# Kernel tuning notes

Measured on AMD Instinct MI355X. Metric: run time of the kernel, lower is better.

The kernel has to match this reference:

```python
import jax, jax.numpy as jnp
import numpy as np


def _pe(x, y, D):
    # 2D sinusoidal encoding: x in upper half, y in lower half, interleaved sin/cos.
    i = jnp.arange(D // 4, dtype=jnp.float32)
    f = 0.0001 ** (4.0 * i / D)  # (D/4,)

    def half(v):
        a = v[..., None] * f  # (..., D/4)
        return jnp.stack([jnp.sin(a), jnp.cos(a)], axis=-1).reshape(v.shape + (D // 2,))

    return jnp.concatenate([half(x), half(y)], axis=-1)  # (..., D)


def _mlp(x, W1, b1, W2, b2):
    return jax.nn.relu(x @ W1 + b1) @ W2 + b2


def setup_inputs() -> dict:
    key = jax.random.key(0)
    ks = jax.random.split(key, 9)
    B, C, H, S, D = 1024, 64, 21, 3, 1024
    P = S * S * C  # 576
    NS, NSF, NG = 32, 8, 16

    def lin(k, fan_in, fan_out):
        lim = 1.0 / np.sqrt(fan_in)
        return jax.random.uniform(k, (fan_in, fan_out), minval=-lim, maxval=lim, dtype=jnp.float32)

    return {
        "maps": jax.random.normal(ks[0], (B, C, H, H), dtype=jnp.float32),
        "shipyards": jax.random.uniform(ks[1], (B, NS, NSF), dtype=jnp.float32) * 21.0,
        "game_stats": jax.random.normal(ks[2], (B, NG), dtype=jnp.float32),
        "Wp1": lin(ks[3], P, D), "bp1": jnp.zeros((D,), jnp.float32),
        "Wp2": lin(ks[4], D, D), "bp2": jnp.zeros((D,), jnp.float32),
        "Ws1": lin(ks[5], NSF, D), "bs1": jnp.zeros((D,), jnp.float32),
        "Ws2": lin(ks[6], D, D), "bs2": jnp.zeros((D,), jnp.float32),
        "Wg1": lin(ks[7], NG, D), "bg1": jnp.zeros((D,), jnp.float32),
        "Wg2": lin(ks[8], D, D), "bg2": jnp.zeros((D,), jnp.float32),
    }


def reference(maps, shipyards, game_stats, Wp1, bp1, Wp2, bp2,
              Ws1, bs1, Ws2, bs2, Wg1, bg1, Wg2, bg2):
    B, C, H, W = maps.shape
    s = 3  # patch_width
    h, w = H // s, W // s
    D = Wp2.shape[1]
    # Rearrange 'b c (h s1) (w s2) -> b (h w) (s1 s2 c)'
    patches = maps.reshape(B, C, h, s, w, s).transpose(0, 2, 4, 3, 5, 1).reshape(B, h * w, s * s * C)
    emb_p = _mlp(patches, Wp1, bp1, Wp2, bp2)  # (B, 49, D)
    # patch centers: x = 3h+1 (row), y = 3w+1 (col), flattened h-major
    hi, wi = jnp.meshgrid(jnp.arange(h), jnp.arange(w), indexing="ij")
    px = (s * hi + 1).reshape(-1).astype(jnp.float32)
    py = (s * wi + 1).reshape(-1).astype(jnp.float32)
    emb_p = emb_p + _pe(px, py, D)
    emb_s = _mlp(shipyards, Ws1, bs1, Ws2, bs2)  # (B, NS, D)
    # original uses batch element 0's coords for all batches
    emb_s = emb_s + _pe(shipyards[0, :, 0], shipyards[0, :, 1], D)
    emb_g = _mlp(game_stats, Wg1, bg1, Wg2, bg2)[:, None, :]  # (B, 1, D)
    return jnp.concatenate([emb_s, emb_g, emb_p], axis=1)
```

## Files before the change

kernel.cpp:

```cpp
#include <hip/hip_runtime.h>
#include <stdint.h>

typedef __attribute__((ext_vector_type(8))) short bf16x8;
typedef __attribute__((ext_vector_type(4))) float f32x4;

__device__ __forceinline__ unsigned short f2bf(float f) {
  union { float f; uint32_t u; } v; v.f = f;
  uint32_t r = (v.u + 0x7fffu + ((v.u >> 16) & 1u)) >> 16;
  return (unsigned short)r;
}

__device__ __forceinline__ void async16(const void* g, void* l) {
  __builtin_amdgcn_global_load_lds(
      (const __attribute__((address_space(1))) void*)(uintptr_t)g,
      (__attribute__((address_space(3))) void*)(uint32_t)(uintptr_t)l,
      16, 0, 0);
}

__global__ __launch_bounds__(256) void transpose_bf16(
    const float* __restrict__ in, unsigned short* __restrict__ out, int N, int K) {
  __shared__ float tile[32][33];
  int tx = threadIdx.x & 31, ty = threadIdx.x >> 5;
  int n0 = blockIdx.x * 32, k0 = blockIdx.y * 32;
#pragma unroll
  for (int i = 0; i < 32; i += 8)
    tile[ty + i][tx] = in[(size_t)(k0 + ty + i) * N + n0 + tx];
  __syncthreads();
#pragma unroll
  for (int i = 0; i < 32; i += 8)
    out[(size_t)(n0 + ty + i) * K + k0 + tx] = f2bf(tile[tx][ty + i]);
}

__global__ __launch_bounds__(256) void gather_patches(
    const float* __restrict__ maps, unsigned short* __restrict__ P) {
  int bh = blockIdx.x;
  int b = bh / 7, h = bh % 7;
  __shared__ float lds[4032];
  const float* mb = maps + (size_t)b * 64 * 441;
  for (int f = threadIdx.x; f < 4032; f += 256) {
    int c = f / 63, rem = f % 63;
    int s1 = rem / 21, y = rem % 21;
    lds[f] = mb[(size_t)c * 441 + (3 * h + s1) * 21 + y];
  }
  __syncthreads();
  unsigned short* pb = P + ((size_t)b * 49 + (size_t)h * 7) * 576;
#pragma unroll
  for (int w = 0; w < 7; ++w) {
    for (int ep = threadIdx.x; ep < 288; ep += 256) {
      int e = ep * 2;
      int c = e & 63, s2 = (e >> 6) % 3, s1 = e / 192;
      float v0 = lds[c * 63 + s1 * 21 + 3 * w + s2];
      float v1 = lds[(c + 1) * 63 + s1 * 21 + 3 * w + s2];
      ushort2 o; o.x = f2bf(v0); o.y = f2bf(v1);
      *(ushort2*)(pb + (size_t)w * 576 + e) = o;
    }
  }
}

__global__ __launch_bounds__(256) void mlp1_small(
    const float* __restrict__ X, const float* __restrict__ W1,
    const float* __restrict__ b1, unsigned short* __restrict__ H, int K) {
  int t = threadIdx.x;
  size_t r0 = (size_t)blockIdx.x * 16;
  float4 bias = ((const float4*)b1)[t];
  float acc[16][4];
#pragma unroll
  for (int rr = 0; rr < 16; ++rr) {
    acc[rr][0] = bias.x; acc[rr][1] = bias.y; acc[rr][2] = bias.z; acc[rr][3] = bias.w;
  }
  for (int k = 0; k < K; ++k) {
    float4 w = ((const float4*)(W1 + (size_t)k * 1024))[t];
#pragma unroll
    for (int rr = 0; rr < 16; ++rr) {
      float x = X[(r0 + rr) * K + k];
      acc[rr][0] = fmaf(x, w.x, acc[rr][0]);
      acc[rr][1] = fmaf(x, w.y, acc[rr][1]);
      acc[rr][2] = fmaf(x, w.z, acc[rr][2]);
      acc[rr][3] = fmaf(x, w.w, acc[rr][3]);
    }
  }
#pragma unroll
  for (int rr = 0; rr < 16; ++rr) {
    ushort4 o;
    o.x = f2bf(fmaxf(acc[rr][0], 0.0f));
    o.y = f2bf(fmaxf(acc[rr][1], 0.0f));
    o.z = f2bf(fmaxf(acc[rr][2], 0.0f));
    o.w = f2bf(fmaxf(acc[rr][3], 0.0f));
    *(ushort4*)(H + (r0 + rr) * 1024 + 4 * t) = o;
  }
}

__global__ __launch_bounds__(256) void pe_kernel(
    const float* __restrict__ sy, float* __restrict__ pep, float* __restrict__ pes) {
  int r = blockIdx.x, i = threadIdx.x;
  float f = powf(1.0e-4f, (4.0f * (float)i) / 1024.0f);
  float x, y; float* dst;
  if (r < 49) {
    x = (float)(3 * (r / 7) + 1); y = (float)(3 * (r % 7) + 1);
    dst = pep + (size_t)r * 1024;
  } else {
    int s = r - 49;
    x = sy[s * 8 + 0]; y = sy[s * 8 + 1];
    dst = pes + (size_t)s * 1024;
  }
  float sx, cx, syv, cyv;
  sincosf(x * f, &sx, &cx);
  sincosf(y * f, &syv, &cyv);
  dst[2 * i] = sx; dst[2 * i + 1] = cx;
  dst[512 + 2 * i] = syv; dst[512 + 2 * i + 1] = cyv;
}

__global__ __launch_bounds__(512, 2) void gemm256(
    const unsigned short* __restrict__ A, const unsigned short* __restrict__ Bt,
    const float* __restrict__ bias, const float* __restrict__ pe,
    unsigned short* __restrict__ outb, float* __restrict__ outf,
    int M, int K, int mode, int rp, int col_base) {
  __shared__ __align__(16) char lds[3][32768];
  const int t = threadIdx.x;
  const int wave = t >> 6, lane = t & 63;
  const int l15 = lane & 15, quad = lane >> 4;
  const int wm = wave >> 2, wn = wave & 3;

  const int nbx = gridDim.x;
  const int nwg = nbx * gridDim.y;
  const int orig = blockIdx.y * nbx + blockIdx.x;
  const int q = nwg >> 3, r8 = nwg & 7;
  const int xcd = orig & 7, off = orig >> 3;
  const int wg = (xcd < r8 ? xcd * (q + 1) : r8 * (q + 1) + (xcd - r8) * q) + off;
  const int bn = wg % nbx, bm = wg / nbx;

  const size_t rA0 = (size_t)bm * 256;
  const size_t rB0 = (size_t)bn * 256;

  const int ke = (((t & 3) ^ ((t >> 3) & 3)) * 8);
  const unsigned short* pA = A + (rA0 + (t >> 2)) * (size_t)K + ke;
  const unsigned short* pB = Bt + (rB0 + (t >> 2)) * (size_t)K + ke;

  const int aoff0 = (wm * 128 + l15) * 64;
  const int boff0 = (wn * 64 + l15) * 64;
  const int kx = ((quad ^ ((l15 >> 1) & 3)) << 4);

  const int NT = K >> 5;
  f32x4 acc[8][4] = {};

  async16(pA, lds[0] + wave * 1024);
  async16(pA + (size_t)128 * K, lds[0] + 8192 + wave * 1024);
  async16(pB, lds[0] + 16384 + wave * 1024);
  async16(pB + (size_t)128 * K, lds[0] + 24576 + wave * 1024);
  if (NT > 1) {
    async16(pA + 32, lds[1] + wave * 1024);
    async16(pA + (size_t)128 * K + 32, lds[1] + 8192 + wave * 1024);
    async16(pB + 32, lds[1] + 16384 + wave * 1024);
    async16(pB + (size_t)128 * K + 32, lds[1] + 24576 + wave * 1024);
    asm volatile("s_waitcnt vmcnt(4)" ::: "memory");
  } else {
    asm volatile("s_waitcnt vmcnt(0)" ::: "memory");
  }
  __builtin_amdgcn_s_barrier();

  int bc = 0;
  for (int tt = 0; tt < NT; ++tt) {
    const char* La = lds[bc];
    const char* Lb = La + 16384;
    int bs = bc + 2; if (bs >= 3) bs -= 3;
    const bool pf = (tt + 2) < NT;
    const int kt = (tt + 2) << 5;

    bf16x8 av[4], bv[4];
#pragma unroll
    for (int i = 0; i < 4; ++i)
      av[i] = *(const bf16x8*)(La + aoff0 + i * 1024 + kx);
#pragma unroll
    for (int j = 0; j < 4; ++j)
      bv[j] = *(const bf16x8*)(Lb + boff0 + j * 1024 + kx);
    if (pf) {
      async16(pA + kt, lds[bs] + wave * 1024);
      async16(pA + (size_t)128 * K + kt, lds[bs] + 8192 + wave * 1024);
    }
    __builtin_amdgcn_s_barrier();
    __builtin_amdgcn_s_setprio(1);
#pragma unroll
    for (int i = 0; i < 4; ++i)
#pragma unroll
      for (int j = 0; j < 4; ++j)
        acc[i][j] = __builtin_amdgcn_mfma_f32_16x16x32_bf16(av[i], bv[j], acc[i][j], 0, 0, 0);
    __builtin_amdgcn_s_setprio(0);
    __builtin_amdgcn_s_barrier();

    bf16x8 aw[4];
#pragma unroll
    for (int i = 0; i < 4; ++i)
      aw[i] = *(const bf16x8*)(La + aoff0 + (4 + i) * 1024 + kx);
    if (pf) {
      async16(pB + kt, lds[bs] + 16384 + wave * 1024);
      async16(pB + (size_t)128 * K + kt, lds[bs] + 24576 + wave * 1024);
    }
    __builtin_amdgcn_s_barrier();
    __builtin_amdgcn_s_setprio(1);
#pragma unroll
    for (int i = 0; i < 4; ++i)
#pragma unroll
      for (int j = 0; j < 4; ++j)
        acc[4 + i][j] = __builtin_amdgcn_mfma_f32_16x16x32_bf16(aw[i], bv[j], acc[4 + i][j], 0, 0, 0);
    __builtin_amdgcn_s_setprio(0);
    if (pf) asm volatile("s_waitcnt vmcnt(4)" ::: "memory");
    else    asm volatile("s_waitcnt vmcnt(0)" ::: "memory");
    __builtin_amdgcn_s_barrier();
    bc = bc + 1; if (bc >= 3) bc = 0;
  }

  const int gc0 = bn * 256 + wn * 64 + l15;
  float bs4[4];
#pragma unroll
  for (int j = 0; j < 4; ++j) bs4[j] = bias[gc0 + j * 16];

  if (mode == 0) {
#pragma unroll
    for (int i = 0; i < 8; ++i) {
      int gr0 = bm * 256 + wm * 128 + i * 16 + quad * 4;
#pragma unroll
      for (int r = 0; r < 4; ++r) {
        size_t row = (size_t)(gr0 + r);
#pragma unroll
        for (int j = 0; j < 4; ++j) {
          float v = acc[i][j][r] + bs4[j];
          outb[row * 1024 + gc0 + j * 16] = f2bf(fmaxf(v, 0.0f));
        }
      }
    }
  } else {
#pragma unroll
    for (int i = 0; i < 8; ++i) {
      int gr0 = bm * 256 + wm * 128 + i * 16 + quad * 4;
#pragma unroll
      for (int r = 0; r < 4; ++r) {
        int row = gr0 + r;
        int bb = row / rp;
        int p = row - bb * rp;
        size_t orow = (size_t)bb * 82 + (size_t)col_base + (size_t)p;
#pragma unroll
        for (int j = 0; j < 4; ++j) {
          float v = acc[i][j][r] + bs4[j];
          if (pe) v += pe[(size_t)p * 1024 + gc0 + j * 16];
          outf[orow * 1024 + gc0 + j * 16] = v;
        }
      }
    }
  }
}

extern "C" void kernel_launch(void* const* d_in, const int* in_sizes, int n_in,
                              void* d_out, int out_size, void* d_ws, size_t ws_size,
                              hipStream_t stream) {
  const float* maps = (const float*)d_in[0];
  const float* sy   = (const float*)d_in[1];
  const float* gs   = (const float*)d_in[2];
  const float* Wp1  = (const float*)d_in[3];
  const float* bp1  = (const float*)d_in[4];
  const float* Wp2  = (const float*)d_in[5];
  const float* bp2  = (const float*)d_in[6];
  const float* Ws1  = (const float*)d_in[7];
  const float* bs1  = (const float*)d_in[8];
  const float* Ws2  = (const float*)d_in[9];
  const float* bs2  = (const float*)d_in[10];
  const float* Wg1  = (const float*)d_in[11];
  const float* bg1  = (const float*)d_in[12];
  const float* Wg2  = (const float*)d_in[13];
  const float* bg2  = (const float*)d_in[14];
  float* out = (float*)d_out;

  const int B  = in_sizes[0] / (64 * 21 * 21);
  const int Mp = B * 49;
  const int Ms = B * 32;
  const int Mg = B;

  char* p = (char*)d_ws;
  auto alloc = [&](size_t bytes) { char* r = p; p += (bytes + 255) & ~(size_t)255; return r; };
  unsigned short* pat  = (unsigned short*)alloc((size_t)Mp * 576 * 2);
  unsigned short* hp   = (unsigned short*)alloc((size_t)Mp * 1024 * 2);
  unsigned short* hs   = (unsigned short*)alloc((size_t)Ms * 1024 * 2);
  unsigned short* hg   = (unsigned short*)alloc((size_t)Mg * 1024 * 2);
  unsigned short* wp1t = (unsigned short*)alloc((size_t)1024 * 576 * 2);
  unsigned short* wp2t = (unsigned short*)alloc((size_t)1024 * 1024 * 2);
  unsigned short* ws2t = (unsigned short*)alloc((size_t)1024 * 1024 * 2);
  unsigned short* wg2t = (unsigned short*)alloc((size_t)1024 * 1024 * 2);
  float* pep = (float*)alloc((size_t)49 * 1024 * 4);
  float* pes = (float*)alloc((size_t)32 * 1024 * 4);

  transpose_bf16<<<dim3(1024 / 32, 576 / 32), 256, 0, stream>>>(Wp1, wp1t, 1024, 576);
  transpose_bf16<<<dim3(32, 32), 256, 0, stream>>>(Wp2, wp2t, 1024, 1024);
  transpose_bf16<<<dim3(32, 32), 256, 0, stream>>>(Ws2, ws2t, 1024, 1024);
  transpose_bf16<<<dim3(32, 32), 256, 0, stream>>>(Wg2, wg2t, 1024, 1024);

  gather_patches<<<B * 7, 256, 0, stream>>>(maps, pat);

  mlp1_small<<<Ms / 16, 256, 0, stream>>>(sy, Ws1, bs1, hs, 8);
  mlp1_small<<<Mg / 16, 256, 0, stream>>>(gs, Wg1, bg1, hg, 16);

  pe_kernel<<<81, 256, 0, stream>>>(sy, pep, pes);

  gemm256<<<dim3(4, Mp / 256), 512, 0, stream>>>(pat, wp1t, bp1, nullptr, hp, nullptr, Mp, 576, 0, 0, 0);
  gemm256<<<dim3(4, Mp / 256), 512, 0, stream>>>(hp, wp2t, bp2, pep, nullptr, out, Mp, 1024, 1, 49, 33);
  gemm256<<<dim3(4, Ms / 256), 512, 0, stream>>>(hs, ws2t, bs2, pes, nullptr, out, Ms, 1024, 1, 32, 0);
  gemm256<<<dim3(4, Mg / 256), 512, 0, stream>>>(hg, wg2t, bg2, nullptr, nullptr, out, Mg, 1024, 1, 1, 32);

  (void)n_in; (void)out_size; (void)ws_size;
}
```

Baseline: 871.6 us.

## Fuse preprocessing into one kernel and group second-layer GEMMs into one launch

Merges the four weight transposes, the patch gather, the two small first-layer MLPs and the positional-encoding kernel into a single block-dispatched prep kernel. The three second-layer GEMMs become one grouped launch with a shared XCD swizzle, and the GEMM mode becomes a template parameter. This cuts the launch count from twelve to three and lets small GEMMs fill the idle CUs left by the big one. The patch gather now writes ushort4 instead of ushort2. In exchange, the prep kernel has branchy per-block dispatch and a union LDS allocation sized for the largest role.

Measured after the change: 815.8 us. 1.07x faster.

```diff
diff --git a/kernel.cpp b/kernel.cpp
--- a/kernel.cpp
+++ b/kernel.cpp
@@ -17,51 +17,39 @@
       16, 0, 0);
 }
 
-__global__ __launch_bounds__(256) void transpose_bf16(
-    const float* __restrict__ in, unsigned short* __restrict__ out, int N, int K) {
-  __shared__ float tile[32][33];
-  int tx = threadIdx.x & 31, ty = threadIdx.x >> 5;
-  int n0 = blockIdx.x * 32, k0 = blockIdx.y * 32;
-#pragma unroll
-  for (int i = 0; i < 32; i += 8)
-    tile[ty + i][tx] = in[(size_t)(k0 + ty + i) * N + n0 + tx];
-  __syncthreads();
-#pragma unroll
-  for (int i = 0; i < 32; i += 8)
-    out[(size_t)(n0 + ty + i) * K + k0 + tx] = f2bf(tile[tx][ty + i]);
-}
-
-__global__ __launch_bounds__(256) void gather_patches(
-    const float* __restrict__ maps, unsigned short* __restrict__ P) {
-  int bh = blockIdx.x;
-  int b = bh / 7, h = bh % 7;
-  __shared__ float lds[4032];
-  const float* mb = maps + (size_t)b * 64 * 441;
+union PrepLds { float gbuf[4032]; float tile[32][33]; };
+
+__device__ __forceinline__ void gather_body(PrepLds& u, const float* __restrict__ maps,
+                                            unsigned short* __restrict__ pat, int b) {
+  int b0 = b / 7, h = b % 7;
+  const float* mb = maps + (size_t)b0 * 64 * 441;
   for (int f = threadIdx.x; f < 4032; f += 256) {
     int c = f / 63, rem = f % 63;
     int s1 = rem / 21, y = rem % 21;
-    lds[f] = mb[(size_t)c * 441 + (3 * h + s1) * 21 + y];
+    u.gbuf[f] = mb[(size_t)c * 441 + (3 * h + s1) * 21 + y];
   }
   __syncthreads();
-  unsigned short* pb = P + ((size_t)b * 49 + (size_t)h * 7) * 576;
-#pragma unroll
-  for (int w = 0; w < 7; ++w) {
-    for (int ep = threadIdx.x; ep < 288; ep += 256) {
-      int e = ep * 2;
-      int c = e & 63, s2 = (e >> 6) % 3, s1 = e / 192;
-      float v0 = lds[c * 63 + s1 * 21 + 3 * w + s2];
-      float v1 = lds[(c + 1) * 63 + s1 * 21 + 3 * w + s2];
-      ushort2 o; o.x = f2bf(v0); o.y = f2bf(v1);
-      *(ushort2*)(pb + (size_t)w * 576 + e) = o;
-    }
-  }
-}
-
-__global__ __launch_bounds__(256) void mlp1_small(
-    const float* __restrict__ X, const float* __restrict__ W1,
-    const float* __restrict__ b1, unsigned short* __restrict__ H, int K) {
+  unsigned short* pb = pat + ((size_t)b0 * 49 + (size_t)h * 7) * 576;
+  for (int idx = threadIdx.x; idx < 1008; idx += 256) {
+    int w = idx / 144, ep = idx - w * 144;
+    int e = ep * 4;
+    int c = e & 63, s2 = (e >> 6) % 3, s1 = e / 192;
+    int base = c * 63 + s1 * 21 + 3 * w + s2;
+    ushort4 o;
+    o.x = f2bf(u.gbuf[base]);
+    o.y = f2bf(u.gbuf[base + 63]);
+    o.z = f2bf(u.gbuf[base + 126]);
+    o.w = f2bf(u.gbuf[base + 189]);
+    *(ushort4*)(pb + (size_t)w * 576 + e) = o;
+  }
+}
+
+__device__ __forceinline__ void mlp1_body(const float* __restrict__ X,
+                                          const float* __restrict__ W1,
+                                          const float* __restrict__ b1,
+                                          unsigned short* __restrict__ H,
+                                          int K, size_t r0) {
   int t = threadIdx.x;
-  size_t r0 = (size_t)blockIdx.x * 16;
   float4 bias = ((const float4*)b1)[t];
   float acc[16][4];
 #pragma unroll
@@ -90,9 +78,23 @@
   }
 }
 
-__global__ __launch_bounds__(256) void pe_kernel(
-    const float* __restrict__ sy, float* __restrict__ pep, float* __restrict__ pes) {
-  int r = blockIdx.x, i = threadIdx.x;
+__device__ __forceinline__ void transpose_body(PrepLds& u, const float* __restrict__ in,
+                                               unsigned short* __restrict__ out,
+                                               int N, int K, int n0, int k0) {
+  int tx = threadIdx.x & 31, ty = threadIdx.x >> 5;
+#pragma unroll
+  for (int i = 0; i < 32; i += 8)
+    u.tile[ty + i][tx] = in[(size_t)(k0 + ty + i) * N + n0 + tx];
+  __syncthreads();
+#pragma unroll
+  for (int i = 0; i < 32; i += 8)
+    out[(size_t)(n0 + ty + i) * K + k0 + tx] = f2bf(u.tile[tx][ty + i]);
+}
+
+__device__ __forceinline__ void pe_body(const float* __restrict__ sy,
+                                        float* __restrict__ pep, float* __restrict__ pes,
+                                        int r) {
+  int i = threadIdx.x;
   float f = powf(1.0e-4f, (4.0f * (float)i) / 1024.0f);
   float x, y; float* dst;
   if (r < 49) {
@@ -110,25 +112,46 @@
   dst[512 + 2 * i] = syv; dst[512 + 2 * i + 1] = cyv;
 }
 
-__global__ __launch_bounds__(512, 2) void gemm256(
+__global__ __launch_bounds__(256) void prep_kernel(
+    const float* maps, unsigned short* pat,
+    const float* sy, const float* Ws1, const float* bs1, unsigned short* hs,
+    const float* gs, const float* Wg1, const float* bg1, unsigned short* hg,
+    const float* Wp1, unsigned short* wp1t, const float* Wp2, unsigned short* wp2t,
+    const float* Ws2, unsigned short* ws2t, const float* Wg2, unsigned short* wg2t,
+    float* pep, float* pes, int B) {
+  __shared__ PrepLds u;
+  int b = blockIdx.x, n;
+  n = B * 7;
+  if (b < n) { gather_body(u, maps, pat, b); return; }
+  b -= n;
+  n = B * 2;
+  if (b < n) { mlp1_body(sy, Ws1, bs1, hs, 8, (size_t)b * 16); return; }
+  b -= n;
+  n = B / 16;
+  if (b < n) { mlp1_body(gs, Wg1, bg1, hg, 16, (size_t)b * 16); return; }
+  b -= n;
+  if (b < 576) { transpose_body(u, Wp1, wp1t, 1024, 576, (b & 31) * 32, (b >> 5) * 32); return; }
+  b -= 576;
+  if (b < 1024) { transpose_body(u, Wp2, wp2t, 1024, 1024, (b & 31) * 32, (b >> 5) * 32); return; }
+  b -= 1024;
+  if (b < 1024) { transpose_body(u, Ws2, ws2t, 1024, 1024, (b & 31) * 32, (b >> 5) * 32); return; }
+  b -= 1024;
+  if (b < 1024) { transpose_body(u, Wg2, wg2t, 1024, 1024, (b & 31) * 32, (b >> 5) * 32); return; }
+  b -= 1024;
+  pe_body(sy, pep, pes, b);
+}
+
+template <int MODE>
+__device__ __forceinline__ void gemm_body(char* lds0, int idx,
     const unsigned short* __restrict__ A, const unsigned short* __restrict__ Bt,
     const float* __restrict__ bias, const float* __restrict__ pe,
     unsigned short* __restrict__ outb, float* __restrict__ outf,
-    int M, int K, int mode, int rp, int col_base) {
-  __shared__ __align__(16) char lds[3][32768];
+    int K, int rp, int col_base) {
   const int t = threadIdx.x;
   const int wave = t >> 6, lane = t & 63;
   const int l15 = lane & 15, quad = lane >> 4;
   const int wm = wave >> 2, wn = wave & 3;
-
-  const int nbx = gridDim.x;
-  const int nwg = nbx * gridDim.y;
-  const int orig = blockIdx.y * nbx + blockIdx.x;
-  const int q = nwg >> 3, r8 = nwg & 7;
-  const int xcd = orig & 7, off = orig >> 3;
-  const int wg = (xcd < r8 ? xcd * (q + 1) : r8 * (q + 1) + (xcd - r8) * q) + off;
-  const int bn = wg % nbx, bm = wg / nbx;
-
+  const int bn = idx & 3, bm = idx >> 2;
   const size_t rA0 = (size_t)bm * 256;
   const size_t rB0 = (size_t)bn * 256;
 
@@ -143,15 +166,15 @@
   const int NT = K >> 5;
   f32x4 acc[8][4] = {};
 
-  async16(pA, lds[0] + wave * 1024);
-  async16(pA + (size_t)128 * K, lds[0] + 8192 + wave * 1024);
-  async16(pB, lds[0] + 16384 + wave * 1024);
-  async16(pB + (size_t)128 * K, lds[0] + 24576 + wave * 1024);
+  async16(pA, lds0 + wave * 1024);
+  async16(pA + (size_t)128 * K, lds0 + 8192 + wave * 1024);
+  async16(pB, lds0 + 16384 + wave * 1024);
+  async16(pB + (size_t)128 * K, lds0 + 24576 + wave * 1024);
   if (NT > 1) {
-    async16(pA + 32, lds[1] + wave * 1024);
-    async16(pA + (size_t)128 * K + 32, lds[1] + 8192 + wave * 1024);
-    async16(pB + 32, lds[1] + 16384 + wave * 1024);
-    async16(pB + (size_t)128 * K + 32, lds[1] + 24576 + wave * 1024);
+    async16(pA + 32, lds0 + 32768 + wave * 1024);
+    async16(pA + (size_t)128 * K + 32, lds0 + 32768 + 8192 + wave * 1024);
+    async16(pB + 32, lds0 + 32768 + 16384 + wave * 1024);
+    async16(pB + (size_t)128 * K + 32, lds0 + 32768 + 24576 + wave * 1024);
     asm volatile("s_waitcnt vmcnt(4)" ::: "memory");
   } else {
     asm volatile("s_waitcnt vmcnt(0)" ::: "memory");
@@ -160,9 +183,10 @@
 
   int bc = 0;
   for (int tt = 0; tt < NT; ++tt) {
-    const char* La = lds[bc];
+    const char* La = lds0 + bc * 32768;
     const char* Lb = La + 16384;
     int bs = bc + 2; if (bs >= 3) bs -= 3;
+    char* Ls = lds0 + bs * 32768;
     const bool pf = (tt + 2) < NT;
     const int kt = (tt + 2) << 5;
 
@@ -174,8 +198,8 @@
     for (int j = 0; j < 4; ++j)
       bv[j] = *(const bf16x8*)(Lb + boff0 + j * 1024 + kx);
     if (pf) {
-      async16(pA + kt, lds[bs] + wave * 1024);
-      async16(pA + (size_t)128 * K + kt, lds[bs] + 8192 + wave * 1024);
+      async16(pA + kt, Ls + wave * 1024);
+      async16(pA + (size_t)128 * K + kt, Ls + 8192 + wave * 1024);
     }
     __builtin_amdgcn_s_barrier();
     __builtin_amdgcn_s_setprio(1);
@@ -192,8 +216,8 @@
     for (int i = 0; i < 4; ++i)
       aw[i] = *(const bf16x8*)(La + aoff0 + (4 + i) * 1024 + kx);
     if (pf) {
-      async16(pB + kt, lds[bs] + 16384 + wave * 1024);
-      async16(pB + (size_t)128 * K + kt, lds[bs] + 24576 + wave * 1024);
+      async16(pB + kt, Ls + 16384 + wave * 1024);
+      async16(pB + (size_t)128 * K + kt, Ls + 24576 + wave * 1024);
     }
     __builtin_amdgcn_s_barrier();
     __builtin_amdgcn_s_setprio(1);
@@ -214,7 +238,7 @@
 #pragma unroll
   for (int j = 0; j < 4; ++j) bs4[j] = bias[gc0 + j * 16];
 
-  if (mode == 0) {
+  if (MODE == 0) {
 #pragma unroll
     for (int i = 0; i < 8; ++i) {
       int gr0 = bm * 256 + wm * 128 + i * 16 + quad * 4;
@@ -247,6 +271,38 @@
       }
     }
   }
+}
+
+__device__ __forceinline__ int xcd_swizzle(int orig, int nwg) {
+  int q = nwg >> 3, r8 = nwg & 7;
+  int xcd = orig & 7, off = orig >> 3;
+  return (xcd < r8 ? xcd * (q + 1) : r8 * (q + 1) + (xcd - r8) * q) + off;
+}
+
+__global__ __launch_bounds__(512, 2) void gemm_l1(
+    const unsigned short* __restrict__ A, const unsigned short* __restrict__ Bt,
+    const float* __restrict__ bias, unsigned short* __restrict__ outb,
+    int K, int nwg) {
+  __shared__ __align__(16) char lds[3][32768];
+  int wg = xcd_swizzle(blockIdx.x, nwg);
+  gemm_body<0>(&lds[0][0], wg, A, Bt, bias, nullptr, outb, nullptr, K, 0, 0);
+}
+
+struct G3 {
+  const unsigned short* A[3];
+  const unsigned short* Bt[3];
+  const float* bias[3];
+  const float* pe[3];
+  int K[3], rp[3], cb[3], bstart[3];
+};
+
+__global__ __launch_bounds__(512, 2) void gemm_l2(G3 g, float* __restrict__ out, int nwg) {
+  __shared__ __align__(16) char lds[3][32768];
+  int wg = xcd_swizzle(blockIdx.x, nwg);
+  int grp = (wg >= g.bstart[2]) ? 2 : (wg >= g.bstart[1] ? 1 : 0);
+  int idx = wg - g.bstart[grp];
+  gemm_body<1>(&lds[0][0], idx, g.A[grp], g.Bt[grp], g.bias[grp], g.pe[grp],
+               nullptr, out, g.K[grp], g.rp[grp], g.cb[grp]);
 }
 
 extern "C" void kernel_launch(void* const* d_in, const int* in_sizes, int n_in,
@@ -287,22 +343,26 @@
   float* pep = (float*)alloc((size_t)49 * 1024 * 4);
   float* pes = (float*)alloc((size_t)32 * 1024 * 4);
 
-  transpose_bf16<<<dim3(1024 / 32, 576 / 32), 256, 0, stream>>>(Wp1, wp1t, 1024, 576);
-  transpose_bf16<<<dim3(32, 32), 256, 0, stream>>>(Wp2, wp2t, 1024, 1024);
-  transpose_bf16<<<dim3(32, 32), 256, 0, stream>>>(Ws2, ws2t, 1024, 1024);
-  transpose_bf16<<<dim3(32, 32), 256, 0, stream>>>(Wg2, wg2t, 1024, 1024);
-
-  gather_patches<<<B * 7, 256, 0, stream>>>(maps, pat);
-
-  mlp1_small<<<Ms / 16, 256, 0, stream>>>(sy, Ws1, bs1, hs, 8);
-  mlp1_small<<<Mg / 16, 256, 0, stream>>>(gs, Wg1, bg1, hg, 16);
-
-  pe_kernel<<<81, 256, 0, stream>>>(sy, pep, pes);
-
-  gemm256<<<dim3(4, Mp / 256), 512, 0, stream>>>(pat, wp1t, bp1, nullptr, hp, nullptr, Mp, 576, 0, 0, 0);
-  gemm256<<<dim3(4, Mp / 256), 512, 0, stream>>>(hp, wp2t, bp2, pep, nullptr, out, Mp, 1024, 1, 49, 33);
-  gemm256<<<dim3(4, Ms / 256), 512, 0, stream>>>(hs, ws2t, bs2, pes, nullptr, out, Ms, 1024, 1, 32, 0);
-  gemm256<<<dim3(4, Mg / 256), 512, 0, stream>>>(hg, wg2t, bg2, nullptr, nullptr, out, Mg, 1024, 1, 1, 32);
+  int prep_blocks = B * 7 + B * 2 + B / 16 + 576 + 3 * 1024 + 81;
+  prep_kernel<<<prep_blocks, 256, 0, stream>>>(
+      maps, pat, sy, Ws1, bs1, hs, gs, Wg1, bg1, hg,
+      Wp1, wp1t, Wp2, wp2t, Ws2, ws2t, Wg2, wg2t, pep, pes, B);
+
+  int nwg1 = (Mp / 256) * 4;
+  gemm_l1<<<nwg1, 512, 0, stream>>>(pat, wp1t, bp1, hp, 576, nwg1);
+
+  G3 g;
+  g.A[0] = hp;   g.Bt[0] = wp2t; g.bias[0] = bp2; g.pe[0] = pep;
+  g.K[0] = 1024; g.rp[0] = 49;   g.cb[0] = 33;
+  g.A[1] = hs;   g.Bt[1] = ws2t; g.bias[1] = bs2; g.pe[1] = pes;
+  g.K[1] = 1024; g.rp[1] = 32;   g.cb[1] = 0;
+  g.A[2] = hg;   g.Bt[2] = wg2t; g.bias[2] = bg2; g.pe[2] = nullptr;
+  g.K[2] = 1024; g.rp[2] = 1;    g.cb[2] = 32;
+  int n2 = (Mp / 256) * 4;
+  int n3 = n2 + (Ms / 256) * 4;
+  int nwg2 = n3 + (Mg / 256) * 4;
+  g.bstart[0] = 0; g.bstart[1] = n2; g.bstart[2] = n3;
+  gemm_l2<<<nwg2, 512, 0, stream>>>(g, out, nwg2);
 
   (void)n_in; (void)out_size; (void)ws_size;
 }
```
